# Kernel tuning notes

Hardware: AMD Instinct MI355X
Metric: run time of the kernel (lower is better)

The kernel has to match this reference:

```python
import jax, jax.numpy as jnp
import numpy as np


def setup_inputs() -> dict:
    key = jax.random.key(0)
    k1, k2, k3 = jax.random.split(key, 3)
    shape = (1, 48, 64, 128, 1)  # [B, D/4, H/4, W/4, C=1] cost volume
    return {
        "c1": jax.random.normal(k1, shape, dtype=jnp.float32),
        "c2": jax.random.normal(k2, shape, dtype=jnp.float32),
        "c3": jax.random.normal(k3, shape, dtype=jnp.float32),
    }


def _regress(c):
    # UpSampling3D(4): nearest-neighbor repeat along D, H, W -> [B, D, H, W, 1]
    x = jnp.repeat(jnp.repeat(jnp.repeat(c, 4, axis=1), 4, axis=2), 4, axis=3)
    # all-ones 4x4x4 box filter, stride 1, SAME padding (TF pads lo=1, hi=2;
    # lax 'SAME' matches this split for even kernels)
    filt = jnp.ones((4, 4, 4, 1, 1), dtype=x.dtype)  # DHWIO
    x = jax.lax.conv_general_dilated(
        x, filt, window_strides=(1, 1, 1), padding="SAME",
        dimension_numbers=("NDHWC", "DHWIO", "NDHWC"))
    x = jnp.squeeze(x, -1)  # [B, D, H, W]
    # soft-argmin over disparity axis
    w = jax.nn.softmax(x, axis=1)
    disp = jnp.arange(x.shape[1], dtype=x.dtype)[None, :, None, None]
    return jnp.sum(w * disp, axis=1)  # [B, H, W]


def reference(c1, c2, c3):
    # inference path (training=None): only c3 is processed
    return _regress(c3)
```

## Files before the change

### kernel.cpp

```cpp
#include <hip/hip_runtime.h>


#define DC 48
#define HC 64
#define WC 128
#define WOUT 512
#define HOUT 256
#define NPIX (HOUT * WOUT)
#define LOG2E 1.4426950408889634f

__device__ __forceinline__ void axis_weights(int p, int& off, float& w0, float& w1) {
    off = (p == 0) ? -1 : 0;
    w0  = (p == 0) ? 1.f : (p == 1) ? 4.f : (p == 2) ? 3.f : 2.f;
    w1  = (p == 0) ? 3.f : (p == 1) ? 0.f : (p == 2) ? 1.f : 2.f;
}

__global__ __launch_bounds__(256)
void regress_kernel(const float* __restrict__ c3, float* __restrict__ out) {
    int lane = threadIdx.x & 63;
    int px   = lane & 15;
    int q    = lane >> 4;
    int wv   = threadIdx.x >> 6;
    int g    = blockIdx.x * 64 + wv * 16 + px;

    int w = g & (WOUT - 1);
    int h = g >> 9;

    int jh = h >> 2, ph = h & 3;
    int jw = w >> 2, pw = w & 3;

    int offh, offw;
    float whA, whB, wwA, wwB;
    axis_weights(ph, offh, whA, whB);
    axis_weights(pw, offw, wwA, wwB);

    int jh0 = jh + offh, jh1 = jh0 + 1;
    float wh0 = (jh0 >= 0 && jh0 < HC) ? whA : 0.f;
    float wh1 = (jh1 < HC) ? whB : 0.f;
    jh0 = (jh0 < 0) ? 0 : jh0;
    jh1 = (jh1 > HC - 1) ? HC - 1 : jh1;

    int jw0 = jw + offw, jw1 = jw0 + 1;
    float ww0 = (jw0 >= 0 && jw0 < WC) ? wwA : 0.f;
    float ww1 = (jw1 < WC) ? wwB : 0.f;
    jw0 = (jw0 < 0) ? 0 : jw0;
    jw1 = (jw1 > WC - 1) ? WC - 1 : jw1;

    float w00 = wh0 * ww0 * LOG2E, w01 = wh0 * ww1 * LOG2E;
    float w10 = wh1 * ww0 * LOG2E, w11 = wh1 * ww1 * LOG2E;

    int i00 = jh0 * WC + jw0, i01 = jh0 * WC + jw1;
    int i10 = jh1 * WC + jw0, i11 = jh1 * WC + jw1;

    int base = 12 * q;
    float S[14];
    #pragma unroll
    for (int kk = 0; kk < 14; ++kk) {
        int jd  = base - 1 + kk;
        bool ok = (jd >= 0) && (jd < DC);
        int jc  = ok ? jd : 0;
        const float* p = c3 + jc * (HC * WC);
        float val = w00 * p[i00] + w01 * p[i01] + w10 * p[i10] + w11 * p[i11];
        S[kk] = ok ? val : 0.f;
    }

    float m = -1e30f;
    #pragma unroll
    for (int i = 0; i < 12; ++i) {
        float Sm = S[i], Sc = S[i + 1], Sp = S[i + 2];
        float x0 = Sm + 3.f * Sc;
        float x1 = 4.f * Sc;
        float x2 = 3.f * Sc + Sp;
        float x3 = 2.f * Sc + 2.f * Sp;
        m = fmaxf(m, fmaxf(fmaxf(x0, x1), fmaxf(x2, x3)));
    }
    m = fmaxf(m, __shfl_xor(m, 16, 64));
    m = fmaxf(m, __shfl_xor(m, 32, 64));

    float s = 0.f, sd = 0.f;
    #pragma unroll
    for (int i = 0; i < 12; ++i) {
        float Sm = S[i], Sc = S[i + 1], Sp = S[i + 2];
        float x0 = Sm + 3.f * Sc;
        float x1 = 4.f * Sc;
        float x2 = 3.f * Sc + Sp;
        float x3 = 2.f * Sc + 2.f * Sp;
        float e0 = __builtin_amdgcn_exp2f(x0 - m);
        float e1 = __builtin_amdgcn_exp2f(x1 - m);
        float e2 = __builtin_amdgcn_exp2f(x2 - m);
        float e3 = __builtin_amdgcn_exp2f(x3 - m);
        s += e0 + e1 + e2 + e3;
        float d0 = (float)(4 * (base + i));
        sd = fmaf(e0, d0, sd);
        sd = fmaf(e1, d0 + 1.f, sd);
        sd = fmaf(e2, d0 + 2.f, sd);
        sd = fmaf(e3, d0 + 3.f, sd);
    }
    s  += __shfl_xor(s, 16, 64);
    s  += __shfl_xor(s, 32, 64);
    sd += __shfl_xor(sd, 16, 64);
    sd += __shfl_xor(sd, 32, 64);

    if (q == 0) out[g] = sd / s;
}

extern "C" void kernel_launch(void* const* d_in, const int* in_sizes, int n_in,
                              void* d_out, int out_size, void* d_ws, size_t ws_size,
                              hipStream_t stream) {
    (void)in_sizes; (void)n_in; (void)d_ws; (void)ws_size; (void)out_size;
    const float* c3 = (const float*)d_in[2];
    float* out = (float*)d_out;
    regress_kernel<<<NPIX / 64, 256, 0, stream>>>(c3, out);
}
```

Baseline: 66.99 us.

## Map lanes to pixels and reduce depth quarters across waves via LDS

Reassigns threads so each wavefront covers 64 consecutive output pixels for one depth quarter, instead of 16 pixels by 4 quarters. The cross-quarter max and sum reductions move from wave shuffles to shared memory with two block barriers. This is meant to widen load and store coalescing per wave, at the cost of LDS traffic and synchronization.

```diff
diff --git a/kernel.cpp b/kernel.cpp
--- a/kernel.cpp
+++ b/kernel.cpp
@@ -17,11 +17,9 @@
 
 __global__ __launch_bounds__(256)
 void regress_kernel(const float* __restrict__ c3, float* __restrict__ out) {
-    int lane = threadIdx.x & 63;
-    int px   = lane & 15;
-    int q    = lane >> 4;
-    int wv   = threadIdx.x >> 6;
-    int g    = blockIdx.x * 64 + wv * 16 + px;
+    int x = threadIdx.x;
+    int q = threadIdx.y;
+    int g = blockIdx.x * 64 + x;
 
     int w = g & (WOUT - 1);
     int h = g >> 9;
@@ -74,8 +72,13 @@
         float x3 = 2.f * Sc + 2.f * Sp;
         m = fmaxf(m, fmaxf(fmaxf(x0, x1), fmaxf(x2, x3)));
     }
-    m = fmaxf(m, __shfl_xor(m, 16, 64));
-    m = fmaxf(m, __shfl_xor(m, 32, 64));
+
+    __shared__ float lm[4][64];
+    __shared__ float ls[4][64];
+    __shared__ float lsd[4][64];
+    lm[q][x] = m;
+    __syncthreads();
+    m = fmaxf(fmaxf(lm[0][x], lm[1][x]), fmaxf(lm[2][x], lm[3][x]));
 
     float s = 0.f, sd = 0.f;
     #pragma unroll
@@ -96,12 +99,15 @@
         sd = fmaf(e2, d0 + 2.f, sd);
         sd = fmaf(e3, d0 + 3.f, sd);
     }
-    s  += __shfl_xor(s, 16, 64);
-    s  += __shfl_xor(s, 32, 64);
-    sd += __shfl_xor(sd, 16, 64);
-    sd += __shfl_xor(sd, 32, 64);
 
-    if (q == 0) out[g] = sd / s;
+    ls[q][x]  = s;
+    lsd[q][x] = sd;
+    __syncthreads();
+    if (q == 0) {
+        float st  = (ls[0][x]  + ls[1][x])  + (ls[2][x]  + ls[3][x]);
+        float sdt = (lsd[0][x] + lsd[1][x]) + (lsd[2][x] + lsd[3][x]);
+        out[g] = sdt / st;
+    }
 }
 
 extern "C" void kernel_launch(void* const* d_in, const int* in_sizes, int n_in,
@@ -110,5 +116,5 @@
     (void)in_sizes; (void)n_in; (void)d_ws; (void)ws_size; (void)out_size;
     const float* c3 = (const float*)d_in[2];
     float* out = (float*)d_out;
-    regress_kernel<<<NPIX / 64, 256, 0, stream>>>(c3, out);
+    regress_kernel<<<NPIX / 64, dim3(64, 4), 0, stream>>>(c3, out);
 }
```

Measured after the change: 77.83 us. 1.16x slower.
